# Optimization experiments

Hardware: AMD Instinct MI355X
Metric: run time of the kernel (lower is better)

Reference implementation:

```python
import jax, jax.numpy as jnp
import numpy as np

B, S, H = 16, 512, 768
NH, HD = 12, 64  # num heads, head dim


def setup_inputs() -> dict:
    key = jax.random.key(0)
    ks = jax.random.split(key, 7)
    std = 0.02
    return {
        "hidden_state": jax.random.normal(ks[0], (B, S, H), dtype=jnp.float32),
        "attention_mask": jnp.ones((B, S), dtype=jnp.float32),
        "Wq": jax.random.normal(ks[1], (H, H), dtype=jnp.float32) * std,
        "bq": jnp.zeros((H,), dtype=jnp.float32),
        "Wk": jax.random.normal(ks[2], (H, H), dtype=jnp.float32) * std,
        "bk": jnp.zeros((H,), dtype=jnp.float32),
        "Wv": jax.random.normal(ks[3], (H, H), dtype=jnp.float32) * std,
        "bv": jnp.zeros((H,), dtype=jnp.float32),
    }


def reference(hidden_state, attention_mask, Wq, bq, Wk, bk, Wv, bv):
    b, s, h = hidden_state.shape
    scale = 1.0 / jnp.sqrt(jnp.asarray(HD, hidden_state.dtype))

    def split_heads(x):  # [B,S,H] -> [B,NH,S,HD]
        return x.reshape(b, s, NH, HD).transpose(0, 2, 1, 3)

    q = split_heads(hidden_state @ Wq.T + bq)
    k = split_heads(hidden_state @ Wk.T + bk)
    v = split_heads(hidden_state @ Wv.T + bv)

    # [B,NH,S,S]
    scores = jnp.einsum("bhqd,bhkd->bhqk", q, k) * scale
    mask_add = (1.0 - attention_mask)[:, None, None, :] * -10000.0
    probs = jax.nn.softmax(scores + mask_add, axis=-1)
    # dropout is identity in eval / deterministic reference

    ctx = jnp.einsum("bhqk,bhkd->bhqd", probs, v)
    ctx = ctx.transpose(0, 2, 1, 3).reshape(b, s, NH * HD)
    return ctx, probs
```

## Files before the change

kernel.cpp:

```cpp
#include <hip/hip_runtime.h>

namespace {
constexpr int kB  = 16;
constexpr int kS  = 512;
constexpr int kH  = 768;
constexpr int kNH = 12;
constexpr int kHD = 64;
constexpr int kM  = kB * kS;
}

typedef __attribute__((ext_vector_type(8))) short  short8;
typedef __attribute__((ext_vector_type(4))) float  f32x4;
typedef __attribute__((ext_vector_type(4))) unsigned short us4;
typedef __attribute__((ext_vector_type(2))) unsigned int   u32x2;

__device__ __forceinline__ unsigned short f2bf(float x) {
    unsigned u = __float_as_uint(x);
    return (unsigned short)((u + 0x7FFFu + ((u >> 16) & 1u)) >> 16);
}

__device__ __forceinline__ unsigned pack_bf16(float lo, float hi) {
    return (unsigned)f2bf(lo) | ((unsigned)f2bf(hi) << 16);
}

__device__ __forceinline__ void load_lds16(const unsigned short* g, unsigned short* l) {
    __builtin_amdgcn_global_load_lds(
        (const __attribute__((address_space(1))) void*)g,
        (__attribute__((address_space(3))) void*)l,
        16, 0, 0);
}

__global__ __launch_bounds__(256) void f32_to_bf16_kernel(
    const float* __restrict__ src, unsigned short* __restrict__ dst, int n4)
{
    int i = blockIdx.x * 256 + threadIdx.x;
    if (i >= n4) return;
    float4 v = reinterpret_cast<const float4*>(src)[i];
    us4 o;
    o.x = f2bf(v.x); o.y = f2bf(v.y); o.z = f2bf(v.z); o.w = f2bf(v.w);
    reinterpret_cast<us4*>(dst)[i] = o;
}

__global__ __launch_bounds__(256) void qkv_mfma_kernel(
    const unsigned short* __restrict__ hbf,
    const unsigned short* __restrict__ Wqb,
    const unsigned short* __restrict__ Wkb,
    const unsigned short* __restrict__ Wvb,
    const float* __restrict__ bq, const float* __restrict__ bk,
    const float* __restrict__ bv,
    unsigned short* __restrict__ qhi, unsigned short* __restrict__ qlo,
    unsigned short* __restrict__ khi, unsigned short* __restrict__ klo,
    unsigned short* __restrict__ vt)
{
    const int which = blockIdx.z;
    const unsigned short* W = (which == 0) ? Wqb : (which == 1) ? Wkb : Wvb;
    const float* bias       = (which == 0) ? bq  : (which == 1) ? bk  : bv;

    const int n0 = blockIdx.x * 128;
    const int m0 = blockIdx.y * 128;

    const int t    = threadIdx.x;
    const int lane = t & 63;
    const int w    = t >> 6;
    const int wm   = w >> 1;
    const int wn   = w & 1;

    __shared__ unsigned short As[128 * 32];
    __shared__ unsigned short Bs[128 * 32];

    f32x4 acc[4][4] = {};

    const int srow  = w * 32 + (lane >> 2);
    const int skoff = (lane & 3) * 8;
    const unsigned short* gA0 = hbf + (size_t)(m0 + srow) * kH + skoff;
    const unsigned short* gA1 = gA0 + (size_t)16 * kH;
    const unsigned short* gB0 = W   + (size_t)(n0 + srow) * kH + skoff;
    const unsigned short* gB1 = gB0 + (size_t)16 * kH;
    unsigned short* lA0 = &As[(w * 32) * 32];
    unsigned short* lA1 = &As[(w * 32 + 16) * 32];
    unsigned short* lB0 = &Bs[(w * 32) * 32];
    unsigned short* lB1 = &Bs[(w * 32 + 16) * 32];

    const int frow = lane & 15;
    const int fk   = (lane >> 4) * 8;

    for (int k0 = 0; k0 < kH; k0 += 32) {
        load_lds16(gA0 + k0, lA0);
        load_lds16(gA1 + k0, lA1);
        load_lds16(gB0 + k0, lB0);
        load_lds16(gB1 + k0, lB1);
        __syncthreads();

        short8 af[4], bf[4];
#pragma unroll
        for (int i = 0; i < 4; ++i)
            af[i] = *reinterpret_cast<const short8*>(
                &As[(wm * 64 + i * 16 + frow) * 32 + fk]);
#pragma unroll
        for (int j = 0; j < 4; ++j)
            bf[j] = *reinterpret_cast<const short8*>(
                &Bs[(wn * 64 + j * 16 + frow) * 32 + fk]);
#pragma unroll
        for (int i = 0; i < 4; ++i)
#pragma unroll
            for (int j = 0; j < 4; ++j)
                acc[i][j] = __builtin_amdgcn_mfma_f32_16x16x32_bf16(
                    af[i], bf[j], acc[i][j], 0, 0, 0);
        __syncthreads();
    }

    const int col = lane & 15;
    const int rq4 = (lane >> 4) << 2;

    if (which < 2) {
        unsigned short* ohi = which ? khi : qhi;
        unsigned short* olo = which ? klo : qlo;
#pragma unroll
        for (int j = 0; j < 4; ++j) {
            const int n  = n0 + wn * 64 + j * 16 + col;
            const float bj = bias[n];
            const int hh = n >> 6, d = n & 63;
#pragma unroll
            for (int i = 0; i < 4; ++i) {
                const int mrow = m0 + wm * 64 + i * 16 + rq4;
                const int bb = mrow >> 9;
                const int ss = mrow & 511;
                const size_t base =
                    ((size_t)(bb * kNH + hh) * kS + ss) * kHD + d;
#pragma unroll
                for (int r = 0; r < 4; ++r) {
                    float x = acc[i][j][r] + bj;
                    unsigned short hi = f2bf(x);
                    float res = x - __uint_as_float((unsigned)hi << 16);
                    ohi[base + (size_t)r * kHD] = hi;
                    olo[base + (size_t)r * kHD] = f2bf(res);
                }
            }
        }
    } else {
#pragma unroll
        for (int j = 0; j < 4; ++j) {
            const int n  = n0 + wn * 64 + j * 16 + col;
            const float bj = bias[n];
            const int hh = n >> 6, d = n & 63;
#pragma unroll
            for (int i = 0; i < 4; ++i) {
                const int mrow = m0 + wm * 64 + i * 16 + rq4;
                const int bb = mrow >> 9;
                const int ss = mrow & 511;
                us4 o;
                o.x = f2bf(acc[i][j][0] + bj);
                o.y = f2bf(acc[i][j][1] + bj);
                o.z = f2bf(acc[i][j][2] + bj);
                o.w = f2bf(acc[i][j][3] + bj);
                *reinterpret_cast<us4*>(
                    &vt[((size_t)(bb * kNH + hh) * kHD + d) * kS + ss]) = o;
            }
        }
    }
}

__global__ __launch_bounds__(256) void attn_kernel(
    const unsigned short* __restrict__ qhi, const unsigned short* __restrict__ qlo,
    const unsigned short* __restrict__ khi, const unsigned short* __restrict__ klo,
    const unsigned short* __restrict__ vtp, const float* __restrict__ mask,
    float* __restrict__ ctx, float* __restrict__ probs)
{
    const int bid = blockIdx.x;
    const int swz = (bid & 7) * 192 + (bid >> 3);
    const int qt  = swz & 7;
    const int bh  = swz >> 3;
    const int b   = bh / kNH;
    const int h   = bh % kNH;
    const int q0  = qt * 64;

    const int t    = threadIdx.x;
    const int lane = t & 63;
    const int w    = t >> 6;
    const int g    = lane >> 4;
    const int fr   = lane & 15;

    __shared__ unsigned short Khs[4096];
    __shared__ unsigned short Kls[4096];
    __shared__ unsigned short Vts[4096];
    __shared__ unsigned int   Pp[4][576];

    const int qrow = q0 + w * 16 + fr;
    const unsigned short* qh = qhi + ((size_t)bh * kS + qrow) * kHD + g * 8;
    const unsigned short* ql = qlo + ((size_t)bh * kS + qrow) * kHD + g * 8;
    const short8 qfh0 = *reinterpret_cast<const short8*>(qh);
    const short8 qfh1 = *reinterpret_cast<const short8*>(qh + 32);
    const short8 qfl0 = *reinterpret_cast<const short8*>(ql);
    const short8 qfl1 = *reinterpret_cast<const short8*>(ql + 32);

    const int c0 = (w * 2 + 0) * 64 + lane;
    const int c1 = (w * 2 + 1) * 64 + lane;
    const int r0 = c0 >> 3, r1 = c1 >> 3;
    const int s0b = ((c0 & 7) * 16) ^ ((r0 & 7) << 4);
    const int s1b = ((c1 & 7) * 16) ^ ((r1 & 7) << 4);
    const int ko0 = r0 * 128 + s0b,  ko1 = r1 * 128 + s1b;
    const int vo0 = r0 * 1024 + s0b, vo1 = r1 * 1024 + s1b;
    const char* kh_b = (const char*)(khi + (size_t)bh * kS * kHD);
    const char* kl_b = (const char*)(klo + (size_t)bh * kS * kHD);
    const char* vt_b = (const char*)(vtp + (size_t)bh * kHD * kS);
    unsigned short* ldsK0 = &Khs[(w * 2 + 0) * 512];
    unsigned short* ldsK1 = &Khs[(w * 2 + 1) * 512];
    unsigned short* ldsL0 = &Kls[(w * 2 + 0) * 512];
    unsigned short* ldsL1 = &Kls[(w * 2 + 1) * 512];
    unsigned short* ldsV0 = &Vts[(w * 2 + 0) * 512];
    unsigned short* ldsV1 = &Vts[(w * 2 + 1) * 512];

    unsigned pk[8][4][2];
    f32x4 cacc[4] = {};
    float rs = 0.0f;
    const float* mrow = mask + b * kS;

#pragma unroll
    for (int kt = 0; kt < 8; ++kt) {
        load_lds16((const unsigned short*)(kh_b + kt * 8192 + ko0), ldsK0);
        load_lds16((const unsigned short*)(kh_b + kt * 8192 + ko1), ldsK1);
        load_lds16((const unsigned short*)(kl_b + kt * 8192 + ko0), ldsL0);
        load_lds16((const unsigned short*)(kl_b + kt * 8192 + ko1), ldsL1);
        load_lds16((const unsigned short*)(vt_b + kt * 128 + vo0), ldsV0);
        load_lds16((const unsigned short*)(vt_b + kt * 128 + vo1), ldsV1);
        __syncthreads();

#pragma unroll
        for (int ks = 0; ks < 4; ++ks) {
            f32x4 sa = {};
#pragma unroll
            for (int d2 = 0; d2 < 2; ++d2) {
                const int kr  = ks * 16 + fr;
                const int off = kr * 128 + ((d2 * 64 + g * 16) ^ ((kr & 7) << 4));
                short8 ah = *reinterpret_cast<const short8*>((const char*)Khs + off);
                short8 al = *reinterpret_cast<const short8*>((const char*)Kls + off);
                const short8 qhf = d2 ? qfh1 : qfh0;
                const short8 qlf = d2 ? qfl1 : qfl0;
                sa = __builtin_amdgcn_mfma_f32_16x16x32_bf16(ah, qhf, sa, 0, 0, 0);
                sa = __builtin_amdgcn_mfma_f32_16x16x32_bf16(ah, qlf, sa, 0, 0, 0);
                sa = __builtin_amdgcn_mfma_f32_16x16x32_bf16(al, qhf, sa, 0, 0, 0);
            }
            const float4 mv = *reinterpret_cast<const float4*>(
                &mrow[kt * 64 + ks * 16 + g * 4]);
            float p0 = __expf(fmaf(sa[0], 0.125f, fmaf(mv.x, 1e4f, -1e4f)));
            float p1 = __expf(fmaf(sa[1], 0.125f, fmaf(mv.y, 1e4f, -1e4f)));
            float p2 = __expf(fmaf(sa[2], 0.125f, fmaf(mv.z, 1e4f, -1e4f)));
            float p3 = __expf(fmaf(sa[3], 0.125f, fmaf(mv.w, 1e4f, -1e4f)));
            rs += (p0 + p1) + (p2 + p3);
            const unsigned u0 = pack_bf16(p0, p1);
            const unsigned u1 = pack_bf16(p2, p3);
            pk[kt][ks][0] = u0;
            pk[kt][ks][1] = u1;
            *reinterpret_cast<u32x2*>(&Pp[w][fr * 36 + ks * 8 + g * 2]) =
                (u32x2){u0, u1};
        }

#pragma unroll
        for (int kp = 0; kp < 2; ++kp) {
            short8 pa = *reinterpret_cast<const short8*>(
                &Pp[w][fr * 36 + kp * 16 + g * 4]);
#pragma unroll
            for (int dt = 0; dt < 4; ++dt) {
                const int vr  = dt * 16 + fr;
                const int off = vr * 128 + ((kp * 64 + g * 16) ^ ((vr & 7) << 4));
                short8 vb = *reinterpret_cast<const short8*>((const char*)Vts + off);
                cacc[dt] = __builtin_amdgcn_mfma_f32_16x16x32_bf16(
                    pa, vb, cacc[dt], 0, 0, 0);
            }
        }
        __syncthreads();
    }

    rs += __shfl_xor(rs, 16, 64);
    rs += __shfl_xor(rs, 32, 64);
    const float inv = 1.0f / rs;

    float* prow = probs + ((size_t)bh * kS + qrow) * kS;
#pragma unroll
    for (int kt = 0; kt < 8; ++kt)
#pragma unroll
        for (int ks = 0; ks < 4; ++ks) {
            const unsigned u0 = pk[kt][ks][0], u1 = pk[kt][ks][1];
            f32x4 o;
            o.x = __uint_as_float(u0 << 16) * inv;
            o.y = __uint_as_float(u0 & 0xFFFF0000u) * inv;
            o.z = __uint_as_float(u1 << 16) * inv;
            o.w = __uint_as_float(u1 & 0xFFFF0000u) * inv;
            __builtin_nontemporal_store(
                o, reinterpret_cast<f32x4*>(prow + kt * 64 + ks * 16 + g * 4));
        }

    float invr[4];
#pragma unroll
    for (int r = 0; r < 4; ++r) invr[r] = __shfl(inv, g * 4 + r, 64);
    float* crow = ctx + ((size_t)(b * kS + q0 + w * 16 + g * 4)) * kH
                      + h * kHD + fr;
#pragma unroll
    for (int dt = 0; dt < 4; ++dt)
#pragma unroll
        for (int r = 0; r < 4; ++r)
            __builtin_nontemporal_store(cacc[dt][r] * invr[r],
                                        crow + (size_t)r * kH + dt * 16);
}

extern "C" void kernel_launch(void* const* d_in, const int* in_sizes, int n_in,
                              void* d_out, int out_size, void* d_ws, size_t ws_size,
                              hipStream_t stream) {
    (void)in_sizes; (void)n_in; (void)out_size; (void)ws_size;

    const float* hidden = (const float*)d_in[0];
    const float* mask   = (const float*)d_in[1];
    const float* Wq     = (const float*)d_in[2];
    const float* bq     = (const float*)d_in[3];
    const float* Wk     = (const float*)d_in[4];
    const float* bk     = (const float*)d_in[5];
    const float* Wv     = (const float*)d_in[6];
    const float* bv     = (const float*)d_in[7];

    float* ctx   = (float*)d_out;
    float* probs = (float*)d_out + (size_t)kB * kS * kH;

    unsigned short* hbf = (unsigned short*)d_ws;
    unsigned short* wqb = hbf + (size_t)kM * kH;
    unsigned short* wkb = wqb + (size_t)kH * kH;
    unsigned short* wvb = wkb + (size_t)kH * kH;
    unsigned short* qhi = wvb + (size_t)kH * kH;
    const size_t nqkv = (size_t)kB * kNH * kS * kHD;
    unsigned short* qlo = qhi + nqkv;
    unsigned short* khi = qlo + nqkv;
    unsigned short* klo = khi + nqkv;
    unsigned short* vt  = klo + nqkv;

    const int nh4 = (kM * kH) / 4;
    const int nw4 = (kH * kH) / 4;
    f32_to_bf16_kernel<<<nh4 / 256, 256, 0, stream>>>(hidden, hbf, nh4);
    f32_to_bf16_kernel<<<nw4 / 256, 256, 0, stream>>>(Wq, wqb, nw4);
    f32_to_bf16_kernel<<<nw4 / 256, 256, 0, stream>>>(Wk, wkb, nw4);
    f32_to_bf16_kernel<<<nw4 / 256, 256, 0, stream>>>(Wv, wvb, nw4);

    dim3 gp(kH / 128, kM / 128, 3);
    qkv_mfma_kernel<<<gp, 256, 0, stream>>>(hbf, wqb, wkb, wvb,
                                            bq, bk, bv,
                                            qhi, qlo, khi, klo, vt);

    attn_kernel<<<dim3(kB * kNH * (kS / 64)), 256, 0, stream>>>(
        qhi, qlo, khi, klo, vt, mask, ctx, probs);
}
```

Measured before the change: 399.6 us.

## Double-buffer K/V LDS tiles in attention loop and raise wave priority

Splits the K-high, K-low and V-transposed shared-memory tiles into two buffers. The next key tile's global-to-LDS loads are issued right after the barrier so they overlap the current tile's MFMA and softmax work, and one barrier per iteration is dropped. It also raises the wave priority around the compute section with s_setprio. The cost is roughly double the LDS for K/V, which may lower occupancy per CU.

New measurement: 399.0 us. About the same (-0.2%).

```diff
diff --git a/kernel.cpp b/kernel.cpp
--- a/kernel.cpp
+++ b/kernel.cpp
@@ -180,9 +180,9 @@
     const int g    = lane >> 4;
     const int fr   = lane & 15;
 
-    __shared__ unsigned short Khs[4096];
-    __shared__ unsigned short Kls[4096];
-    __shared__ unsigned short Vts[4096];
+    __shared__ unsigned short Khs[2][4096];
+    __shared__ unsigned short Kls[2][4096];
+    __shared__ unsigned short Vts[2][4096];
     __shared__ unsigned int   Pp[4][576];
 
     const int qrow = q0 + w * 16 + fr;
@@ -203,27 +203,37 @@
     const char* kh_b = (const char*)(khi + (size_t)bh * kS * kHD);
     const char* kl_b = (const char*)(klo + (size_t)bh * kS * kHD);
     const char* vt_b = (const char*)(vtp + (size_t)bh * kHD * kS);
-    unsigned short* ldsK0 = &Khs[(w * 2 + 0) * 512];
-    unsigned short* ldsK1 = &Khs[(w * 2 + 1) * 512];
-    unsigned short* ldsL0 = &Kls[(w * 2 + 0) * 512];
-    unsigned short* ldsL1 = &Kls[(w * 2 + 1) * 512];
-    unsigned short* ldsV0 = &Vts[(w * 2 + 0) * 512];
-    unsigned short* ldsV1 = &Vts[(w * 2 + 1) * 512];
+    const int l0 = (w * 2 + 0) * 512;
+    const int l1 = (w * 2 + 1) * 512;
 
     unsigned pk[8][4][2];
     f32x4 cacc[4] = {};
     float rs = 0.0f;
     const float* mrow = mask + b * kS;
 
+    load_lds16((const unsigned short*)(kh_b + ko0), &Khs[0][l0]);
+    load_lds16((const unsigned short*)(kh_b + ko1), &Khs[0][l1]);
+    load_lds16((const unsigned short*)(kl_b + ko0), &Kls[0][l0]);
+    load_lds16((const unsigned short*)(kl_b + ko1), &Kls[0][l1]);
+    load_lds16((const unsigned short*)(vt_b + vo0), &Vts[0][l0]);
+    load_lds16((const unsigned short*)(vt_b + vo1), &Vts[0][l1]);
+
 #pragma unroll
     for (int kt = 0; kt < 8; ++kt) {
-        load_lds16((const unsigned short*)(kh_b + kt * 8192 + ko0), ldsK0);
-        load_lds16((const unsigned short*)(kh_b + kt * 8192 + ko1), ldsK1);
-        load_lds16((const unsigned short*)(kl_b + kt * 8192 + ko0), ldsL0);
-        load_lds16((const unsigned short*)(kl_b + kt * 8192 + ko1), ldsL1);
-        load_lds16((const unsigned short*)(vt_b + kt * 128 + vo0), ldsV0);
-        load_lds16((const unsigned short*)(vt_b + kt * 128 + vo1), ldsV1);
+        const int cur = kt & 1;
         __syncthreads();
+
+        if (kt < 7) {
+            const int nxt = cur ^ 1;
+            load_lds16((const unsigned short*)(kh_b + (kt + 1) * 8192 + ko0), &Khs[nxt][l0]);
+            load_lds16((const unsigned short*)(kh_b + (kt + 1) * 8192 + ko1), &Khs[nxt][l1]);
+            load_lds16((const unsigned short*)(kl_b + (kt + 1) * 8192 + ko0), &Kls[nxt][l0]);
+            load_lds16((const unsigned short*)(kl_b + (kt + 1) * 8192 + ko1), &Kls[nxt][l1]);
+            load_lds16((const unsigned short*)(vt_b + (kt + 1) * 128 + vo0), &Vts[nxt][l0]);
+            load_lds16((const unsigned short*)(vt_b + (kt + 1) * 128 + vo1), &Vts[nxt][l1]);
+        }
+
+        __builtin_amdgcn_s_setprio(1);
 
 #pragma unroll
         for (int ks = 0; ks < 4; ++ks) {
@@ -232,8 +242,8 @@
             for (int d2 = 0; d2 < 2; ++d2) {
                 const int kr  = ks * 16 + fr;
                 const int off = kr * 128 + ((d2 * 64 + g * 16) ^ ((kr & 7) << 4));
-                short8 ah = *reinterpret_cast<const short8*>((const char*)Khs + off);
-                short8 al = *reinterpret_cast<const short8*>((const char*)Kls + off);
+                short8 ah = *reinterpret_cast<const short8*>((const char*)Khs[cur] + off);
+                short8 al = *reinterpret_cast<const short8*>((const char*)Kls[cur] + off);
                 const short8 qhf = d2 ? qfh1 : qfh0;
                 const short8 qlf = d2 ? qfl1 : qfl0;
                 sa = __builtin_amdgcn_mfma_f32_16x16x32_bf16(ah, qhf, sa, 0, 0, 0);
@@ -263,12 +273,13 @@
             for (int dt = 0; dt < 4; ++dt) {
                 const int vr  = dt * 16 + fr;
                 const int off = vr * 128 + ((kp * 64 + g * 16) ^ ((vr & 7) << 4));
-                short8 vb = *reinterpret_cast<const short8*>((const char*)Vts + off);
+                short8 vb = *reinterpret_cast<const short8*>((const char*)Vts[cur] + off);
                 cacc[dt] = __builtin_amdgcn_mfma_f32_16x16x32_bf16(
                     pa, vb, cacc[dt], 0, 0, 0);
             }
         }
-        __syncthreads();
+
+        __builtin_amdgcn_s_setprio(0);
     }
 
     rs += __shfl_xor(rs, 16, 64);
```
